# Kernel tuning notes

Hardware: AMD Instinct MI355X
Metric: run time of the kernel (lower is better)

Reference implementation:

```python
import jax, jax.numpy as jnp
import numpy as np

# ---- cfg constants (JDE / YOLOv4-tracking style) ----
STRIDES = (8.0, 16.0, 32.0)
TRAIN_SIZE = 608.0
LEVELS = 3
NUM_ANCHORS = 4
EMB_DIM = 208
CONF_THRESH = 0.5
NMS_IOU = 0.45
K_LEVEL = 300   # proposals kept per level after confidence filtering
MAX_PROP = 500  # final padded proposal count per image
_ANCHORS = np.array([
    [[8, 24], [11, 34], [16, 48], [23, 68]],
    [[32, 96], [45, 135], [64, 192], [90, 271]],
    [[128, 384], [180, 540], [256, 640], [512, 640]],
], dtype=np.float32)  # [LEVELS, NUM_ANCHORS, 2] in pixels


def _decode_level(pred, emb, anchors_px, stride):
    """pred [B,A,H,W,6], emb [B,H,W,E] -> [B, A*H*W, 4+1+E] (xyxy in [0,1], conf, l2-norm emb)."""
    B, A, H, W, _ = pred.shape
    conf = jax.nn.softmax(pred[..., 4:6], axis=-1)[..., 1:2]  # [B,A,H,W,1]
    anc = anchors_px / stride  # anchors in grid units, [A,2]
    gy, gx = jnp.meshgrid(jnp.arange(H, dtype=pred.dtype),
                          jnp.arange(W, dtype=pred.dtype), indexing="ij")
    aw = anc[:, 0][:, None, None]  # [A,1,1]
    ah = anc[:, 1][:, None, None]
    # JDE-style delta decode: offsets scaled by anchor size, exp size decode
    x = pred[..., 0] * aw + gx
    y = pred[..., 1] * ah + gy
    w = jnp.exp(pred[..., 2]) * aw
    h = jnp.exp(pred[..., 3]) * ah
    scale = stride / TRAIN_SIZE  # back to pixels, then normalize by train size
    x1 = jnp.clip((x - 0.5 * w) * scale, 0.0, 1.0)
    y1 = jnp.clip((y - 0.5 * h) * scale, 0.0, 1.0)
    x2 = jnp.clip((x + 0.5 * w) * scale, 0.0, 1.0)
    y2 = jnp.clip((y + 0.5 * h) * scale, 0.0, 1.0)
    box = jnp.stack([x1, y1, x2, y2], axis=-1)  # [B,A,H,W,4]
    # tile embedding over anchors and l2-normalize (tf.math.l2_normalize, eps on sum of squares)
    pe = jnp.broadcast_to(emb[:, None], (B, A, H, W, emb.shape[-1]))
    n2 = jnp.sum(pe * pe, axis=-1, keepdims=True)
    pe = pe * jax.lax.rsqrt(jnp.maximum(n2, 1e-12))
    preds = jnp.concatenate([box, conf, pe], axis=-1)  # [B,A,H,W,4+1+E]
    return preds.reshape(B, A * H * W, preds.shape[-1])


def _conf_topk(props):
    """Confidence threshold + keep top K_LEVEL per image (zero-padded). props [B,N,D]."""
    s = props[..., 4]
    sm = jnp.where(s > CONF_THRESH, s, 0.0)
    top_s, top_i = jax.lax.top_k(sm, K_LEVEL)
    g = jnp.take_along_axis(props, top_i[..., None], axis=1)  # [B,K,D]
    return g * (top_s > 0.0)[..., None].astype(props.dtype)


def _nms_one(props):
    """Greedy NMS for one image. props [N,D] -> [MAX_PROP,D] zero-padded."""
    sc_in = props[:, 4]
    order = jnp.argsort(-sc_in)
    p = props[order]                      # sorted by score desc
    b, sc = p[:, :4], p[:, 4]
    N = b.shape[0]
    area = (b[:, 2] - b[:, 0]) * (b[:, 3] - b[:, 1])
    ix1 = jnp.maximum(b[:, None, 0], b[None, :, 0])
    iy1 = jnp.maximum(b[:, None, 1], b[None, :, 1])
    ix2 = jnp.minimum(b[:, None, 2], b[None, :, 2])
    iy2 = jnp.minimum(b[:, None, 3], b[None, :, 3])
    inter = jnp.clip(ix2 - ix1, 0.0) * jnp.clip(iy2 - iy1, 0.0)
    iou = inter / (area[:, None] + area[None, :] - inter + 1e-9)  # [N,N]
    idxs = jnp.arange(N)
    keep0 = sc > 0.0
    def step(keep, i):
        row = jnp.take(iou, i, axis=0)
        ki = jnp.take(keep, i)
        sup = ki & (row > NMS_IOU) & (idxs > i)
        return keep & jnp.logical_not(sup), None
    keep, _ = jax.lax.scan(step, keep0, idxs)
    keep = keep & (sc > 0.0)
    rank = jnp.cumsum(keep) - 1
    dest = jnp.where(keep & (rank < MAX_PROP), rank, MAX_PROP)  # out-of-range -> dropped
    out = jnp.zeros((MAX_PROP, p.shape[1]), p.dtype).at[dest].set(p, mode="drop")
    return out


def _forward(pred0, pred1, pred2, emb0, emb1, emb2):
    preds = (pred0, pred1, pred2)
    embs = (emb0, emb1, emb2)
    levels = []
    for i in range(LEVELS):
        pr = _decode_level(preds[i], embs[i], jnp.asarray(_ANCHORS[i]), STRIDES[i])
        levels.append(_conf_topk(pr))
    props = jnp.concatenate(levels, axis=1)        # [B, 3*K_LEVEL, 4+1+E]
    out = jax.vmap(_nms_one)(props)                # [B, MAX_PROP, 4+1+E]
    # entry_stop_gradients: grads only through non-zero (valid) entries
    mask = (jnp.sum(out[..., :4], axis=-1) != 0.0).astype(out.dtype)[..., None]
    return out * mask + jax.lax.stop_gradient(out) * (1.0 - mask)


def setup_inputs() -> dict:
    key = jax.random.key(0)
    ks = jax.random.split(key, 6)
    B = 16
    sizes = [76, 38, 19]  # TRAIN_SIZE // stride
    d = {}
    for i, hw in enumerate(sizes):
        d[f"pred{i}"] = jax.random.normal(ks[i], (B, NUM_ANCHORS, hw, hw, 6), jnp.float32)
        d[f"emb{i}"] = jax.random.normal(ks[3 + i], (B, hw, hw, EMB_DIM), jnp.float32)
    return d


def reference(pred0, pred1, pred2, emb0, emb1, emb2):
    return _forward(pred0, pred1, pred2, emb0, emb1, emb2)
```

## Files before the change

### kernel.cpp

```cpp
#include <hip/hip_runtime.h>

typedef unsigned long long u64;
typedef unsigned int u32;

#define KLVL 300
#define NPROP 900
#define MAXPROP 500
#define DDIM 213
#define EDIM 208

__constant__ float c_anc[3][4][2] = {
  {{1.0f, 3.0f}, {1.375f, 4.25f}, {2.0f, 6.0f}, {2.875f, 8.5f}},
  {{2.0f, 6.0f}, {2.8125f, 8.4375f}, {4.0f, 12.0f}, {5.625f, 16.9375f}},
  {{4.0f, 12.0f}, {5.625f, 16.875f}, {8.0f, 20.0f}, {16.0f, 20.0f}},
};
__constant__ float c_scale[3] = { (float)(8.0 / 608.0), (float)(16.0 / 608.0), (float)(32.0 / 608.0) };

__device__ __forceinline__ int level_H(int lvl) { return (lvl == 0) ? 76 : ((lvl == 1) ? 38 : 19); }

#define SB_STRIDE 30336
#define WS_SCORES 0
#define WS_MASK   0
#define MASK_IMG (904*15)
#define WS_SELS (1941504)
#define WS_SELI (WS_SELS + 57600)
#define WS_CNT  (WS_SELI + 57600)
#define WS_BOX  (WS_CNT + 256)
#define BOX_STRIDE 928
#define BOX_IMG (7*928)
#define WS_SRC  (WS_BOX + 415744)

__global__ __launch_bounds__(256) void score_kernel(
    const float* __restrict__ pred0, const float* __restrict__ pred1, const float* __restrict__ pred2,
    float* __restrict__ ws_scores)
{
  const int blk = blockIdx.x;
  const int b = blk / 120;
  const int r = blk % 120;
  int lvl, rb, N, off;
  const float* pred;
  if (r < 91)       { lvl = 0; rb = r;       N = 23104; off = 0;     pred = pred0; }
  else if (r < 114) { lvl = 1; rb = r - 91;  N = 5776;  off = 23104; pred = pred1; }
  else              { lvl = 2; rb = r - 114; N = 1444;  off = 28880; pred = pred2; }
  (void)lvl;
  const int n = rb * 256 + (int)threadIdx.x;
  if (n >= N) return;
  const float* pb = pred + (size_t)b * N * 6;
  float2 l = *reinterpret_cast<const float2*>(pb + (size_t)n * 6 + 4);
  float m = fmaxf(l.x, l.y);
  float e0 = expf(l.x - m), e1 = expf(l.y - m);
  float s = e1 / (e0 + e1);
  ws_scores[(size_t)b * SB_STRIDE + off + n] = (s > 0.5f) ? s : 0.0f;
}

#define TK_T 1024
__global__ __launch_bounds__(TK_T) void select_kernel(
    const float* __restrict__ ws_scores,
    float* __restrict__ sel_score, int* __restrict__ sel_idx, int* __restrict__ cnt)
{
  __shared__ float s_sc[23104];
  __shared__ u32 s_hist[4096];
  __shared__ u32 s_wt[16];
  __shared__ u64 s_wt64[16];
  __shared__ u32 s_sel[4];
  __shared__ float s_selS[KLVL];
  __shared__ int   s_selI[KLVL];

  const int lvl = blockIdx.x % 3;
  const int b = blockIdx.x / 3;
  const int t = threadIdx.x;
  const int lane = t & 63, wid = t >> 6;
  const int H = level_H(lvl);
  const int N = 4 * H * H;
  const int off = (lvl == 0) ? 0 : ((lvl == 1) ? 23104 : 28880);
  const float* gs = ws_scores + (size_t)b * SB_STRIDE + off;

  if (t == 0) s_sel[2] = 0;
  u32 nploc = 0;
  for (int n = t; n < N; n += TK_T) {
    float sm = gs[n];
    s_sc[n] = sm;
    nploc += (sm > 0.0f) ? 1u : 0u;
  }
  __syncthreads();
  if (nploc) atomicAdd(&s_sel[2], nploc);
  __syncthreads();
  const u32 Npos = s_sel[2];
  const bool take_all = (Npos <= (u32)KLVL);
  u32 K = KLVL;
  u32 prefHi = 0, Tkey = 0;

  if (!take_all) {
    for (int pass = 0; pass < 2; ++pass) {
      for (int i = t; i < 4096; i += TK_T) s_hist[i] = 0;
      __syncthreads();
      for (int n = t; n < N; n += TK_T) {
        float v = s_sc[n];
        if (v <= 0.0f) continue;
        u32 key = __float_as_uint(v) - 0x3F000000u;
        if (pass == 0) atomicAdd(&s_hist[key >> 12], 1u);
        else if ((key >> 12) == prefHi) atomicAdd(&s_hist[key & 0xFFFu], 1u);
      }
      __syncthreads();
      const int btop = 4095 - 4 * t;
      u32 h0 = s_hist[btop], h1 = s_hist[btop - 1], h2 = s_hist[btop - 2], h3 = s_hist[btop - 3];
      u32 partial = h0 + h1 + h2 + h3;
      u32 incl = partial;
      #pragma unroll
      for (int off2 = 1; off2 < 64; off2 <<= 1) { u32 v2 = __shfl_up(incl, (unsigned)off2, 64); if (lane >= off2) incl += v2; }
      if (lane == 63) s_wt[wid] = incl;
      __syncthreads();
      u32 above = 0;
      for (int w2 = 0; w2 < wid; ++w2) above += s_wt[w2];
      u32 running = above + incl - partial;
      if (h0 && running < K && K <= running + h0) { s_sel[0] = (u32)(btop);     s_sel[1] = K - running; }
      running += h0;
      if (h1 && running < K && K <= running + h1) { s_sel[0] = (u32)(btop - 1); s_sel[1] = K - running; }
      running += h1;
      if (h2 && running < K && K <= running + h2) { s_sel[0] = (u32)(btop - 2); s_sel[1] = K - running; }
      running += h2;
      if (h3 && running < K && K <= running + h3) { s_sel[0] = (u32)(btop - 3); s_sel[1] = K - running; }
      __syncthreads();
      if (pass == 0) prefHi = s_sel[0];
      else Tkey = (prefHi << 12) | s_sel[0];
      K = s_sel[1];
      __syncthreads();
    }
  }
  const u32 need_ties = take_all ? 0u : K;
  const u32 G = take_all ? Npos : ((u32)KLVL - need_ties);
  const u32 Tbits = Tkey + 0x3F000000u;

  const int chunk = (N + TK_T - 1) / TK_T;
  const int lo = t * chunk;
  const int hi = (lo + chunk < N) ? (lo + chunk) : N;
  u32 cg = 0, ct = 0;
  for (int n = lo; n < hi; ++n) {
    float v = s_sc[n];
    if (v <= 0.0f) continue;
    u32 bits = __float_as_uint(v);
    if (take_all || bits > Tbits) cg++;
    else if (bits == Tbits) ct++;
  }
  u64 pc = ((u64)cg << 32) | (u64)ct;
  u64 incl64 = pc;
  #pragma unroll
  for (int off2 = 1; off2 < 64; off2 <<= 1) { u64 v2 = __shfl_up(incl64, (unsigned)off2, 64); if (lane >= off2) incl64 += v2; }
  if (lane == 63) s_wt64[wid] = incl64;
  __syncthreads();
  u64 ab = 0;
  for (int w2 = 0; w2 < wid; ++w2) ab += s_wt64[w2];
  u64 excl = ab + incl64 - pc;
  u32 g_pos = (u32)(excl >> 32);
  u32 t_pos = (u32)excl;
  for (int n = lo; n < hi; ++n) {
    float v = s_sc[n];
    if (v <= 0.0f) continue;
    u32 bits = __float_as_uint(v);
    if (take_all || bits > Tbits) {
      s_selS[g_pos] = v; s_selI[g_pos] = n; g_pos++;
    } else if (bits == Tbits) {
      if (t_pos < need_ties) { s_selS[G + t_pos] = v; s_selI[G + t_pos] = n; }
      t_pos++;
    }
  }
  __syncthreads();

  const u32 total = take_all ? Npos : (u32)KLVL;
  float* out_s = sel_score + (size_t)b * NPROP + (size_t)lvl * KLVL;
  int* out_i = sel_idx + (size_t)b * NPROP + (size_t)lvl * KLVL;
  if ((u32)t < total) {
    float sv = s_selS[t]; int iv = s_selI[t];
    u32 r = 0;
    for (u32 j = 0; j < total; ++j) {
      float sj = s_selS[j]; int ij = s_selI[j];
      r += ((sj > sv) || (sj == sv && ij < iv)) ? 1u : 0u;
    }
    out_s[r] = sv; out_i[r] = iv;
  }
  for (u32 s2 = total + (u32)t; s2 < (u32)KLVL; s2 += TK_T) { out_s[s2] = 0.0f; out_i[s2] = 0; }
  if (t == 0) cnt[b * 3 + lvl] = (int)total;
}

__global__ __launch_bounds__(1024) void rank_kernel(
    const float* __restrict__ pred0, const float* __restrict__ pred1, const float* __restrict__ pred2,
    const float* __restrict__ sel_score, const int* __restrict__ sel_idx, const int* __restrict__ cnt,
    float* __restrict__ ws_box)
{
  __shared__ float s_sc[NPROP];
  __shared__ int s_ix[NPROP];
  __shared__ int s_c[3];
  const int b = blockIdx.x, t = threadIdx.x;
  if (t < 3) s_c[t] = cnt[b * 3 + t];
  if (t < NPROP) { s_sc[t] = sel_score[(size_t)b * NPROP + t]; s_ix[t] = sel_idx[(size_t)b * NPROP + t]; }
  __syncthreads();
  if (t < NPROP) {
    int lvl = t / KLVL, pos = t - lvl * KLVL;
    if (pos < s_c[lvl]) {
      float sv = s_sc[t];
      u32 rank = (u32)pos;
      for (int ol = 0; ol < 3; ++ol) {
        if (ol == lvl) continue;
        int base = ol * KLVL, co = s_c[ol];
        int lo2 = 0, hi2 = co;
        if (ol < lvl) {
          while (lo2 < hi2) { int mid = (lo2 + hi2) >> 1; if (s_sc[base + mid] >= sv) lo2 = mid + 1; else hi2 = mid; }
        } else {
          while (lo2 < hi2) { int mid = (lo2 + hi2) >> 1; if (s_sc[base + mid] > sv) lo2 = mid + 1; else hi2 = mid; }
        }
        rank += (u32)lo2;
      }
      int n = s_ix[t];
      int Hl = level_H(lvl), HWl = Hl * Hl;
      int a = n / HWl, rem = n - a * HWl, gy = rem / Hl, gx = rem - gy * Hl;
      const float* pred = (lvl == 0) ? pred0 : ((lvl == 1) ? pred1 : pred2);
      const float* p = pred + ((size_t)b * 4 * HWl + (size_t)n) * 6;
      float p0 = p[0], p1 = p[1], p2 = p[2], p3 = p[3];
      float aw = c_anc[lvl][a][0], ah = c_anc[lvl][a][1];
      float x = p0 * aw + (float)gx;
      float y = p1 * ah + (float)gy;
      float wv = expf(p2) * aw;
      float hv = expf(p3) * ah;
      float sc = c_scale[lvl];
      float x1 = fminf(fmaxf((x - 0.5f * wv) * sc, 0.0f), 1.0f);
      float y1 = fminf(fmaxf((y - 0.5f * hv) * sc, 0.0f), 1.0f);
      float x2 = fminf(fmaxf((x + 0.5f * wv) * sc, 0.0f), 1.0f);
      float y2 = fminf(fmaxf((y + 0.5f * hv) * sc, 0.0f), 1.0f);
      float* Bx = ws_box + (size_t)b * BOX_IMG;
      Bx[rank] = x1;
      Bx[BOX_STRIDE + rank] = y1;
      Bx[2 * BOX_STRIDE + rank] = x2;
      Bx[3 * BOX_STRIDE + rank] = y2;
      Bx[4 * BOX_STRIDE + rank] = (x2 - x1) * (y2 - y1);
      Bx[5 * BOX_STRIDE + rank] = sv;
      ((int*)(Bx + 6 * BOX_STRIDE))[rank] = t;
    }
  }
}

__global__ __launch_bounds__(256) void mask_kernel(
    const float* __restrict__ ws_box, const int* __restrict__ cnt, u64* __restrict__ ws_mask)
{
  const int w = blockIdx.x, b = blockIdx.y, t = threadIdx.x;
  const float* B = ws_box + (size_t)b * BOX_IMG;
  const float* X1 = B, * Y1 = B + BOX_STRIDE, * X2 = B + 2 * BOX_STRIDE,
             * Y2 = B + 3 * BOX_STRIDE, * AR = B + 4 * BOX_STRIDE;
  const int Np = cnt[b * 3] + cnt[b * 3 + 1] + cnt[b * 3 + 2];
  __shared__ float jx1[64], jy1[64], jx2[64], jy2[64], jar[64];
  if (t < 64) {
    int j = w * 64 + t;
    if (j < Np) { jx1[t] = X1[j]; jy1[t] = Y1[j]; jx2[t] = X2[j]; jy2[t] = Y2[j]; jar[t] = AR[j]; }
  }
  __syncthreads();
  u64* mk = ws_mask + (size_t)b * MASK_IMG;
  const int jlim = min(64, Np - w * 64);
  for (int i = t; i < Np; i += 256) {
    u64 bits = 0;
    if (i < w * 64 + 63 && jlim > 0) {
      float xi1 = X1[i], yi1 = Y1[i], xi2 = X2[i], yi2 = Y2[i], ai = AR[i];
      for (int jj = 0; jj < jlim; ++jj) {
        int j = w * 64 + jj;
        if (j > i) {
          float xx1 = fmaxf(xi1, jx1[jj]);
          float yy1 = fmaxf(yi1, jy1[jj]);
          float xx2 = fminf(xi2, jx2[jj]);
          float yy2 = fminf(yi2, jy2[jj]);
          float iw = fmaxf(xx2 - xx1, 0.0f);
          float ih = fmaxf(yy2 - yy1, 0.0f);
          float inter = iw * ih;
          float iou = inter / (ai + jar[jj] - inter + 1e-9f);
          if (iou > 0.45f) bits |= (1ull << jj);
        }
      }
    }
    mk[(size_t)i * 15 + w] = bits;
  }
}

__global__ __launch_bounds__(256) void scan_kernel(
    const u64* __restrict__ ws_mask, const int* __restrict__ cnt, int* __restrict__ ws_src)
{
  __shared__ u64 sm[904 * 15];
  __shared__ u64 s_keep[15];
  __shared__ u32 s_pre[16];
  const int b = blockIdx.x, t = threadIdx.x;
  const int Np = cnt[b * 3] + cnt[b * 3 + 1] + cnt[b * 3 + 2];
  const u64* mk = ws_mask + (size_t)b * MASK_IMG;
  for (int i = t; i < Np * 15; i += 256) sm[i] = mk[i];
  __syncthreads();

  if (t < 64) {
    const int lane = t;
    const int lw = (lane < 15) ? lane : 0;
    u64 remv = 0;
    u64 r0 = sm[0 * 15 + lw], r1 = sm[1 * 15 + lw], r2 = sm[2 * 15 + lw], r3 = sm[3 * 15 + lw];
    const int Np4 = Np & ~3;
#define NMS_STEP(ii, rr) { \
      u32 bit_ = (u32)(remv >> ((ii) & 63)) & 1u; \
      u32 sup_ = (u32)__builtin_amdgcn_readlane((int)bit_, (ii) >> 6); \
      if (!sup_) remv |= (rr); }
    for (int i = 0; i < Np4; i += 4) {
      u64 n0 = sm[(size_t)(i + 4) * 15 + lw];
      u64 n1 = sm[(size_t)(i + 5) * 15 + lw];
      u64 n2 = sm[(size_t)(i + 6) * 15 + lw];
      u64 n3 = sm[(size_t)(i + 7) * 15 + lw];
      NMS_STEP(i, r0);
      NMS_STEP(i + 1, r1);
      NMS_STEP(i + 2, r2);
      NMS_STEP(i + 3, r3);
      r0 = n0; r1 = n1; r2 = n2; r3 = n3;
    }
    if (Np4 + 0 < Np) NMS_STEP(Np4 + 0, r0);
    if (Np4 + 1 < Np) NMS_STEP(Np4 + 1, r1);
    if (Np4 + 2 < Np) NMS_STEP(Np4 + 2, r2);
    if (Np4 + 3 < Np) NMS_STEP(Np4 + 3, r3);
#undef NMS_STEP
    if (lane < 15) {
      int base = lane << 6;
      u64 valid = 0;
      if (Np > base) {
        int r = Np - base;
        valid = (r >= 64) ? ~0ull : ((1ull << r) - 1ull);
      }
      s_keep[lane] = (~remv) & valid;
    }
  }
  __syncthreads();
  if (t == 0) {
    u32 run = 0;
    for (int w2 = 0; w2 < 15; ++w2) { s_pre[w2] = run; run += (u32)__popcll(s_keep[w2]); }
  }
  int* src = ws_src + b * MAXPROP;
  for (int r = t; r < MAXPROP; r += 256) src[r] = -1;
  __syncthreads();
  for (int i = t; i < Np; i += 256) {
    u64 kw = s_keep[i >> 6];
    if ((kw >> (i & 63)) & 1ull) {
      u32 rank = s_pre[i >> 6] + (u32)__popcll(kw & ((1ull << (i & 63)) - 1ull));
      if (rank < MAXPROP) src[rank] = i;
    }
  }
}

__global__ __launch_bounds__(256) void out_kernel(
    const float* __restrict__ emb0, const float* __restrict__ emb1, const float* __restrict__ emb2,
    const float* __restrict__ ws_box, const int* __restrict__ ws_src, const int* __restrict__ sel_idx,
    float* __restrict__ out)
{
  const int blk = blockIdx.x;
  const int b = blk / 125;
  const int r = (blk % 125) * 4 + (threadIdx.x >> 6);
  const int lane = threadIdx.x & 63;
  float* orow = out + ((size_t)b * MAXPROP + r) * DDIM;
  const int i = ws_src[b * MAXPROP + r];
  if (i < 0) {
    for (int c = lane; c < DDIM; c += 64) orow[c] = 0.0f;
    return;
  }
  const float* B = ws_box + (size_t)b * BOX_IMG;
  float x1 = B[i], y1 = B[BOX_STRIDE + i], x2 = B[2 * BOX_STRIDE + i], y2 = B[3 * BOX_STRIDE + i];
  float score = B[5 * BOX_STRIDE + i];
  int slot = ((const int*)(B + 6 * BOX_STRIDE))[i];
  int n = sel_idx[(size_t)b * NPROP + slot];
  int lvl = slot / KLVL;
  int Hl = level_H(lvl), HWl = Hl * Hl;
  int a = n / HWl, rem = n - a * HWl, gy = rem / Hl, gx = rem - gy * Hl;
  (void)a;
  const float* emb = (lvl == 0) ? emb0 : ((lvl == 1) ? emb1 : emb2);
  const float* e = emb + ((size_t)(b * Hl + gy) * Hl + gx) * EDIM;
  float v0 = e[lane], v1 = e[lane + 64], v2 = e[lane + 128];
  float v3 = (lane < 16) ? e[lane + 192] : 0.0f;
  float ss = v0 * v0 + v1 * v1 + v2 * v2 + v3 * v3;
  for (int off = 32; off > 0; off >>= 1) ss += __shfl_xor(ss, off, 64);
  float rs = 1.0f / sqrtf(fmaxf(ss, 1e-12f));
  if (lane == 0) {
    orow[0] = x1; orow[1] = y1; orow[2] = x2; orow[3] = y2; orow[4] = score;
  }
  orow[5 + lane] = v0 * rs;
  orow[5 + 64 + lane] = v1 * rs;
  orow[5 + 128 + lane] = v2 * rs;
  if (lane < 16) orow[5 + 192 + lane] = v3 * rs;
}

extern "C" void kernel_launch(void* const* d_in, const int* in_sizes, int n_in,
                              void* d_out, int out_size, void* d_ws, size_t ws_size,
                              hipStream_t stream) {
  const float* pred[3] = {nullptr, nullptr, nullptr};
  const float* emb[3] = {nullptr, nullptr, nullptr};
  for (int i = 0; i < n_in; ++i) {
    const float* p = (const float*)d_in[i];
    switch (in_sizes[i]) {
      case 2217984:  pred[0] = p; break;
      case 554496:   pred[1] = p; break;
      case 138624:   pred[2] = p; break;
      case 19222528: emb[0] = p; break;
      case 4805632:  emb[1] = p; break;
      case 1201408:  emb[2] = p; break;
      default: break;
    }
  }
  char* ws = (char*)d_ws;
  float* ws_scores = (float*)(ws + WS_SCORES);
  u64* ws_mask = (u64*)(ws + WS_MASK);
  float* sel_score = (float*)(ws + WS_SELS);
  int* sel_idx = (int*)(ws + WS_SELI);
  int* cnt = (int*)(ws + WS_CNT);
  float* ws_box = (float*)(ws + WS_BOX);
  int* ws_src = (int*)(ws + WS_SRC);

  score_kernel<<<dim3(1920), dim3(256), 0, stream>>>(pred[0], pred[1], pred[2], ws_scores);
  select_kernel<<<dim3(48), dim3(TK_T), 0, stream>>>(ws_scores, sel_score, sel_idx, cnt);
  rank_kernel<<<dim3(16), dim3(1024), 0, stream>>>(pred[0], pred[1], pred[2], sel_score, sel_idx, cnt, ws_box);
  mask_kernel<<<dim3(15, 16), dim3(256), 0, stream>>>(ws_box, cnt, ws_mask);
  scan_kernel<<<dim3(16), dim3(256), 0, stream>>>(ws_mask, cnt, ws_src);
  out_kernel<<<dim3(2000), dim3(256), 0, stream>>>(emb[0], emb[1], emb[2], ws_box, ws_src, sel_idx, (float*)d_out);
}
```

Before: 270.3 us.

## Replace per-level select with global histogram threshold, collect, and tiled NMS scan

Top-k selection no longer runs in 48 big blocks that each stage a whole level in shared memory. Instead, the score kernel builds a global coarse histogram with atomics, a small kernel finds the threshold bucket, a wide collect kernel gathers candidates, and a sort kernel ranks them. The rank and mask kernels are fused into one, with the mask stored transposed. The NMS scan becomes a single-wave, tile-wise greedy pass using readlane instead of a serial per-box loop. This trades the low-parallelism select and the serial scan for more kernel launches and global atomics, and it depends on capped candidate buffers (512 above the threshold, 1024 tied) that could overflow.

```diff
diff --git a/kernel.cpp b/kernel.cpp
--- a/kernel.cpp
+++ b/kernel.cpp
@@ -19,20 +19,39 @@
 __device__ __forceinline__ int level_H(int lvl) { return (lvl == 0) ? 76 : ((lvl == 1) ? 38 : 19); }
 
 #define SB_STRIDE 30336
-#define WS_SCORES 0
-#define WS_MASK   0
-#define MASK_IMG (904*15)
-#define WS_SELS (1941504)
-#define WS_SELI (WS_SELS + 57600)
-#define WS_CNT  (WS_SELI + 57600)
-#define WS_BOX  (WS_CNT + 256)
+#define MASKT_STRIDE 904
+#define MASK_IMG (15*904)
 #define BOX_STRIDE 928
-#define BOX_IMG (7*928)
-#define WS_SRC  (WS_BOX + 415744)
+#define BOX_IMG (6*928)
+
+#define OFF_SCORES 0
+#define OFF_HIST   1945600
+#define OFF_BUFTS  1945600
+#define OFF_BUFTI  2142208
+#define OFF_BUFGS  2338816
+#define OFF_BUFGI  2437120
+#define OFF_CNTG   2535424
+#define OFF_CNTT   2535680
+#define OFF_THR    2535936
+#define OFF_CNT    2536192
+#define OFF_SELS   2536448
+#define OFF_SELI   2594048
+#define OFF_BOX    2651904
+#define OFF_SRC    3008256
+
+__device__ __forceinline__ u64 readlane_u64(u64 v, int l) {
+  u32 lo = (u32)__builtin_amdgcn_readlane((int)(u32)(v & 0xFFFFFFFFull), l);
+  u32 hi = (u32)__builtin_amdgcn_readlane((int)(u32)(v >> 32), l);
+  return ((u64)hi << 32) | (u64)lo;
+}
+
+__global__ __launch_bounds__(1024) void zero_kernel(u32* __restrict__ h) {
+  h[blockIdx.x * 1024 + threadIdx.x] = 0u;
+}
 
 __global__ __launch_bounds__(256) void score_kernel(
     const float* __restrict__ pred0, const float* __restrict__ pred1, const float* __restrict__ pred2,
-    float* __restrict__ ws_scores)
+    float* __restrict__ ws_scores, u32* __restrict__ hist)
 {
   const int blk = blockIdx.x;
   const int b = blk / 120;
@@ -42,7 +61,6 @@
   if (r < 91)       { lvl = 0; rb = r;       N = 23104; off = 0;     pred = pred0; }
   else if (r < 114) { lvl = 1; rb = r - 91;  N = 5776;  off = 23104; pred = pred1; }
   else              { lvl = 2; rb = r - 114; N = 1444;  off = 28880; pred = pred2; }
-  (void)lvl;
   const int n = rb * 256 + (int)threadIdx.x;
   if (n >= N) return;
   const float* pb = pred + (size_t)b * N * 6;
@@ -50,150 +68,128 @@
   float m = fmaxf(l.x, l.y);
   float e0 = expf(l.x - m), e1 = expf(l.y - m);
   float s = e1 / (e0 + e1);
-  ws_scores[(size_t)b * SB_STRIDE + off + n] = (s > 0.5f) ? s : 0.0f;
-}
-
-#define TK_T 1024
-__global__ __launch_bounds__(TK_T) void select_kernel(
-    const float* __restrict__ ws_scores,
-    float* __restrict__ sel_score, int* __restrict__ sel_idx, int* __restrict__ cnt)
-{
-  __shared__ float s_sc[23104];
-  __shared__ u32 s_hist[4096];
-  __shared__ u32 s_wt[16];
-  __shared__ u64 s_wt64[16];
-  __shared__ u32 s_sel[4];
-  __shared__ float s_selS[KLVL];
-  __shared__ int   s_selI[KLVL];
-
-  const int lvl = blockIdx.x % 3;
-  const int b = blockIdx.x / 3;
-  const int t = threadIdx.x;
-  const int lane = t & 63, wid = t >> 6;
-  const int H = level_H(lvl);
-  const int N = 4 * H * H;
-  const int off = (lvl == 0) ? 0 : ((lvl == 1) ? 23104 : 28880);
-  const float* gs = ws_scores + (size_t)b * SB_STRIDE + off;
-
-  if (t == 0) s_sel[2] = 0;
-  u32 nploc = 0;
-  for (int n = t; n < N; n += TK_T) {
-    float sm = gs[n];
-    s_sc[n] = sm;
-    nploc += (sm > 0.0f) ? 1u : 0u;
-  }
-  __syncthreads();
-  if (nploc) atomicAdd(&s_sel[2], nploc);
-  __syncthreads();
-  const u32 Npos = s_sel[2];
-  const bool take_all = (Npos <= (u32)KLVL);
-  u32 K = KLVL;
-  u32 prefHi = 0, Tkey = 0;
-
-  if (!take_all) {
-    for (int pass = 0; pass < 2; ++pass) {
-      for (int i = t; i < 4096; i += TK_T) s_hist[i] = 0;
-      __syncthreads();
-      for (int n = t; n < N; n += TK_T) {
-        float v = s_sc[n];
-        if (v <= 0.0f) continue;
-        u32 key = __float_as_uint(v) - 0x3F000000u;
-        if (pass == 0) atomicAdd(&s_hist[key >> 12], 1u);
-        else if ((key >> 12) == prefHi) atomicAdd(&s_hist[key & 0xFFFu], 1u);
-      }
-      __syncthreads();
-      const int btop = 4095 - 4 * t;
-      u32 h0 = s_hist[btop], h1 = s_hist[btop - 1], h2 = s_hist[btop - 2], h3 = s_hist[btop - 3];
-      u32 partial = h0 + h1 + h2 + h3;
-      u32 incl = partial;
-      #pragma unroll
-      for (int off2 = 1; off2 < 64; off2 <<= 1) { u32 v2 = __shfl_up(incl, (unsigned)off2, 64); if (lane >= off2) incl += v2; }
-      if (lane == 63) s_wt[wid] = incl;
-      __syncthreads();
-      u32 above = 0;
-      for (int w2 = 0; w2 < wid; ++w2) above += s_wt[w2];
-      u32 running = above + incl - partial;
-      if (h0 && running < K && K <= running + h0) { s_sel[0] = (u32)(btop);     s_sel[1] = K - running; }
-      running += h0;
-      if (h1 && running < K && K <= running + h1) { s_sel[0] = (u32)(btop - 1); s_sel[1] = K - running; }
-      running += h1;
-      if (h2 && running < K && K <= running + h2) { s_sel[0] = (u32)(btop - 2); s_sel[1] = K - running; }
-      running += h2;
-      if (h3 && running < K && K <= running + h3) { s_sel[0] = (u32)(btop - 3); s_sel[1] = K - running; }
-      __syncthreads();
-      if (pass == 0) prefHi = s_sel[0];
-      else Tkey = (prefHi << 12) | s_sel[0];
-      K = s_sel[1];
-      __syncthreads();
+  float sm = (s > 0.5f) ? s : 0.0f;
+  ws_scores[(size_t)b * SB_STRIDE + off + n] = sm;
+  if (sm > 0.0f) {
+    u32 key = __float_as_uint(sm) - 0x3F000000u;
+    u32 bk = min(key >> 12, 2047u);
+    atomicAdd(&hist[(u32)(b * 3 + lvl) * 2048u + bk], 1u);
+  }
+}
+
+__global__ __launch_bounds__(256) void thresh_kernel(
+    const u32* __restrict__ hist, int* __restrict__ thrT, int* __restrict__ cnt,
+    u32* __restrict__ cntG, u32* __restrict__ cntT)
+{
+  __shared__ u32 wt[4];
+  __shared__ int sT;
+  const int bl = blockIdx.x, t = threadIdx.x, lane = t & 63, wid = t >> 6;
+  const u32* h = hist + (size_t)bl * 2048;
+  u32 hv[8]; u32 part = 0;
+  #pragma unroll
+  for (int q = 0; q < 8; ++q) { hv[q] = h[2047 - 8 * t - q]; part += hv[q]; }
+  u32 incl = part;
+  #pragma unroll
+  for (int off = 1; off < 64; off <<= 1) { u32 v = __shfl_up(incl, (unsigned)off, 64); if (lane >= off) incl += v; }
+  if (lane == 63) wt[wid] = incl;
+  __syncthreads();
+  u32 above = 0;
+  for (int w2 = 0; w2 < wid; ++w2) above += wt[w2];
+  const u32 total = wt[0] + wt[1] + wt[2] + wt[3];
+  if (total > 300u) {
+    u32 run = above + incl - part;
+    #pragma unroll
+    for (int q = 0; q < 8; ++q) {
+      u32 hq = hv[q];
+      if (hq && run < 300u && 300u <= run + hq) sT = 2047 - 8 * t - q;
+      run += hq;
     }
   }
-  const u32 need_ties = take_all ? 0u : K;
-  const u32 G = take_all ? Npos : ((u32)KLVL - need_ties);
-  const u32 Tbits = Tkey + 0x3F000000u;
-
-  const int chunk = (N + TK_T - 1) / TK_T;
-  const int lo = t * chunk;
-  const int hi = (lo + chunk < N) ? (lo + chunk) : N;
-  u32 cg = 0, ct = 0;
-  for (int n = lo; n < hi; ++n) {
-    float v = s_sc[n];
-    if (v <= 0.0f) continue;
-    u32 bits = __float_as_uint(v);
-    if (take_all || bits > Tbits) cg++;
-    else if (bits == Tbits) ct++;
-  }
-  u64 pc = ((u64)cg << 32) | (u64)ct;
-  u64 incl64 = pc;
-  #pragma unroll
-  for (int off2 = 1; off2 < 64; off2 <<= 1) { u64 v2 = __shfl_up(incl64, (unsigned)off2, 64); if (lane >= off2) incl64 += v2; }
-  if (lane == 63) s_wt64[wid] = incl64;
-  __syncthreads();
-  u64 ab = 0;
-  for (int w2 = 0; w2 < wid; ++w2) ab += s_wt64[w2];
-  u64 excl = ab + incl64 - pc;
-  u32 g_pos = (u32)(excl >> 32);
-  u32 t_pos = (u32)excl;
-  for (int n = lo; n < hi; ++n) {
-    float v = s_sc[n];
-    if (v <= 0.0f) continue;
-    u32 bits = __float_as_uint(v);
-    if (take_all || bits > Tbits) {
-      s_selS[g_pos] = v; s_selI[g_pos] = n; g_pos++;
-    } else if (bits == Tbits) {
-      if (t_pos < need_ties) { s_selS[G + t_pos] = v; s_selI[G + t_pos] = n; }
-      t_pos++;
-    }
-  }
-  __syncthreads();
-
-  const u32 total = take_all ? Npos : (u32)KLVL;
+  __syncthreads();
+  if (t == 0) {
+    thrT[bl] = (total <= 300u) ? -1 : sT;
+    cnt[bl] = (int)min(total, 300u);
+    cntG[bl] = 0u; cntT[bl] = 0u;
+  }
+}
+
+__global__ __launch_bounds__(256) void collect_kernel(
+    const float* __restrict__ ws_scores, const int* __restrict__ thrT,
+    u32* __restrict__ cntG, u32* __restrict__ cntT,
+    float* __restrict__ bufGs, int* __restrict__ bufGi,
+    float* __restrict__ bufTs, int* __restrict__ bufTi)
+{
+  const int blk = blockIdx.x;
+  const int b = blk / 120;
+  const int r = blk % 120;
+  int lvl, rb, N, off;
+  if (r < 91)       { lvl = 0; rb = r;       N = 23104; off = 0;     }
+  else if (r < 114) { lvl = 1; rb = r - 91;  N = 5776;  off = 23104; }
+  else              { lvl = 2; rb = r - 114; N = 1444;  off = 28880; }
+  const int n = rb * 256 + (int)threadIdx.x;
+  if (n >= N) return;
+  float s = ws_scores[(size_t)b * SB_STRIDE + off + n];
+  if (s <= 0.0f) return;
+  u32 key = __float_as_uint(s) - 0x3F000000u;
+  int bk = (int)min(key >> 12, 2047u);
+  const int bl = b * 3 + lvl;
+  const int T = thrT[bl];
+  if (bk > T) {
+    u32 p = atomicAdd(&cntG[bl], 1u);
+    if (p < 512u) { bufGs[bl * 512 + p] = s; bufGi[bl * 512 + p] = n; }
+  } else if (bk == T) {
+    u32 p = atomicAdd(&cntT[bl], 1u);
+    if (p < 1024u) { bufTs[bl * 1024 + p] = s; bufTi[bl * 1024 + p] = n; }
+  }
+}
+
+__global__ __launch_bounds__(1024) void sort_kernel(
+    const float* __restrict__ bufGs, const int* __restrict__ bufGi,
+    const float* __restrict__ bufTs, const int* __restrict__ bufTi,
+    const u32* __restrict__ cntG, const u32* __restrict__ cntT, const int* __restrict__ cnt,
+    float* __restrict__ sel_score, int* __restrict__ sel_idx)
+{
+  __shared__ float gs[512]; __shared__ int gi[512];
+  __shared__ float ts[1024]; __shared__ int ti[1024];
+  const int bl = blockIdx.x, t = threadIdx.x;
+  const int b = bl / 3, lvl = bl % 3;
+  const int G = (int)min(cntG[bl], 512u);
+  const int Tn = (int)min(cntT[bl], 1024u);
+  const int selCnt = cnt[bl];
+  if (t < G) { gs[t] = bufGs[bl * 512 + t]; gi[t] = bufGi[bl * 512 + t]; }
+  if (t < Tn) { ts[t] = bufTs[bl * 1024 + t]; ti[t] = bufTi[bl * 1024 + t]; }
+  __syncthreads();
   float* out_s = sel_score + (size_t)b * NPROP + (size_t)lvl * KLVL;
   int* out_i = sel_idx + (size_t)b * NPROP + (size_t)lvl * KLVL;
-  if ((u32)t < total) {
-    float sv = s_selS[t]; int iv = s_selI[t];
-    u32 r = 0;
-    for (u32 j = 0; j < total; ++j) {
-      float sj = s_selS[j]; int ij = s_selI[j];
-      r += ((sj > sv) || (sj == sv && ij < iv)) ? 1u : 0u;
-    }
-    out_s[r] = sv; out_i[r] = iv;
-  }
-  for (u32 s2 = total + (u32)t; s2 < (u32)KLVL; s2 += TK_T) { out_s[s2] = 0.0f; out_i[s2] = 0; }
-  if (t == 0) cnt[b * 3 + lvl] = (int)total;
-}
-
-__global__ __launch_bounds__(1024) void rank_kernel(
+  if (t < G) {
+    float sv = gs[t]; int iv = gi[t];
+    int rk = 0;
+    for (int j = 0; j < G; ++j) { float sj = gs[j]; int ij = gi[j]; rk += ((sj > sv) || (sj == sv && ij < iv)) ? 1 : 0; }
+    out_s[rk] = sv; out_i[rk] = iv;
+  }
+  if (t < Tn) {
+    float sv = ts[t]; int iv = ti[t];
+    int rk = 0;
+    for (int j = 0; j < Tn; ++j) { float sj = ts[j]; int ij = ti[j]; rk += ((sj > sv) || (sj == sv && ij < iv)) ? 1 : 0; }
+    if (rk < selCnt - G) { out_s[G + rk] = sv; out_i[G + rk] = iv; }
+  }
+  for (int s2 = selCnt + t; s2 < KLVL; s2 += 1024) { out_s[s2] = 0.0f; out_i[s2] = 0; }
+}
+
+__global__ __launch_bounds__(1024) void rankmask_kernel(
     const float* __restrict__ pred0, const float* __restrict__ pred1, const float* __restrict__ pred2,
     const float* __restrict__ sel_score, const int* __restrict__ sel_idx, const int* __restrict__ cnt,
-    float* __restrict__ ws_box)
+    float* __restrict__ ws_box, u64* __restrict__ ws_mask)
 {
   __shared__ float s_sc[NPROP];
   __shared__ int s_ix[NPROP];
   __shared__ int s_c[3];
+  __shared__ float s_x1[904], s_y1[904], s_x2[904], s_y2[904], s_ar[904];
   const int b = blockIdx.x, t = threadIdx.x;
   if (t < 3) s_c[t] = cnt[b * 3 + t];
   if (t < NPROP) { s_sc[t] = sel_score[(size_t)b * NPROP + t]; s_ix[t] = sel_idx[(size_t)b * NPROP + t]; }
   __syncthreads();
+  const int Np = s_c[0] + s_c[1] + s_c[2];
   if (t < NPROP) {
     int lvl = t / KLVL, pos = t - lvl * KLVL;
     if (pos < s_c[lvl]) {
@@ -231,109 +227,106 @@
       Bx[BOX_STRIDE + rank] = y1;
       Bx[2 * BOX_STRIDE + rank] = x2;
       Bx[3 * BOX_STRIDE + rank] = y2;
-      Bx[4 * BOX_STRIDE + rank] = (x2 - x1) * (y2 - y1);
-      Bx[5 * BOX_STRIDE + rank] = sv;
-      ((int*)(Bx + 6 * BOX_STRIDE))[rank] = t;
+      Bx[4 * BOX_STRIDE + rank] = sv;
+      ((int*)(Bx + 5 * BOX_STRIDE))[rank] = t;
+      s_x1[rank] = x1; s_y1[rank] = y1; s_x2[rank] = x2; s_y2[rank] = y2;
+      s_ar[rank] = (x2 - x1) * (y2 - y1);
     }
   }
-}
-
-__global__ __launch_bounds__(256) void mask_kernel(
-    const float* __restrict__ ws_box, const int* __restrict__ cnt, u64* __restrict__ ws_mask)
-{
-  const int w = blockIdx.x, b = blockIdx.y, t = threadIdx.x;
-  const float* B = ws_box + (size_t)b * BOX_IMG;
-  const float* X1 = B, * Y1 = B + BOX_STRIDE, * X2 = B + 2 * BOX_STRIDE,
-             * Y2 = B + 3 * BOX_STRIDE, * AR = B + 4 * BOX_STRIDE;
-  const int Np = cnt[b * 3] + cnt[b * 3 + 1] + cnt[b * 3 + 2];
-  __shared__ float jx1[64], jy1[64], jx2[64], jy2[64], jar[64];
-  if (t < 64) {
-    int j = w * 64 + t;
-    if (j < Np) { jx1[t] = X1[j]; jy1[t] = Y1[j]; jx2[t] = X2[j]; jy2[t] = Y2[j]; jar[t] = AR[j]; }
-  }
-  __syncthreads();
-  u64* mk = ws_mask + (size_t)b * MASK_IMG;
-  const int jlim = min(64, Np - w * 64);
-  for (int i = t; i < Np; i += 256) {
+  __syncthreads();
+  u64* mkT = ws_mask + (size_t)b * MASK_IMG;
+  const int nW = (Np + 63) >> 6;
+  for (int task = t; task < 15 * 904; task += 1024) {
+    int w = task / 904, i = task - w * 904;
     u64 bits = 0;
-    if (i < w * 64 + 63 && jlim > 0) {
-      float xi1 = X1[i], yi1 = Y1[i], xi2 = X2[i], yi2 = Y2[i], ai = AR[i];
-      for (int jj = 0; jj < jlim; ++jj) {
-        int j = w * 64 + jj;
-        if (j > i) {
-          float xx1 = fmaxf(xi1, jx1[jj]);
-          float yy1 = fmaxf(yi1, jy1[jj]);
-          float xx2 = fminf(xi2, jx2[jj]);
-          float yy2 = fminf(yi2, jy2[jj]);
-          float iw = fmaxf(xx2 - xx1, 0.0f);
-          float ih = fmaxf(yy2 - yy1, 0.0f);
-          float inter = iw * ih;
-          float iou = inter / (ai + jar[jj] - inter + 1e-9f);
-          if (iou > 0.45f) bits |= (1ull << jj);
+    if (i < Np && w < nW) {
+      int j0 = w << 6;
+      int jlim = min(64, Np - j0);
+      if (j0 + 63 > i) {
+        float xi1 = s_x1[i], yi1 = s_y1[i], xi2 = s_x2[i], yi2 = s_y2[i], ai = s_ar[i];
+        for (int jj = 0; jj < jlim; ++jj) {
+          int j = j0 + jj;
+          if (j > i) {
+            float xx1 = fmaxf(xi1, s_x1[j]);
+            float yy1 = fmaxf(yi1, s_y1[j]);
+            float xx2 = fminf(xi2, s_x2[j]);
+            float yy2 = fminf(yi2, s_y2[j]);
+            float iw = fmaxf(xx2 - xx1, 0.0f);
+            float ih = fmaxf(yy2 - yy1, 0.0f);
+            float inter = iw * ih;
+            float iou = inter / (ai + s_ar[j] - inter + 1e-9f);
+            if (iou > 0.45f) bits |= (1ull << jj);
+          }
         }
       }
     }
-    mk[(size_t)i * 15 + w] = bits;
-  }
-}
-
-__global__ __launch_bounds__(256) void scan_kernel(
+    mkT[(size_t)w * MASKT_STRIDE + i] = bits;
+  }
+}
+
+__global__ __launch_bounds__(64) void scan_kernel(
     const u64* __restrict__ ws_mask, const int* __restrict__ cnt, int* __restrict__ ws_src)
 {
-  __shared__ u64 sm[904 * 15];
-  __shared__ u64 s_keep[15];
+  __shared__ u64 s_keep[16];
   __shared__ u32 s_pre[16];
-  const int b = blockIdx.x, t = threadIdx.x;
+  const int b = blockIdx.x;
+  const int lane = (int)threadIdx.x;
   const int Np = cnt[b * 3] + cnt[b * 3 + 1] + cnt[b * 3 + 2];
-  const u64* mk = ws_mask + (size_t)b * MASK_IMG;
-  for (int i = t; i < Np * 15; i += 256) sm[i] = mk[i];
-  __syncthreads();
-
-  if (t < 64) {
-    const int lane = t;
-    const int lw = (lane < 15) ? lane : 0;
-    u64 remv = 0;
-    u64 r0 = sm[0 * 15 + lw], r1 = sm[1 * 15 + lw], r2 = sm[2 * 15 + lw], r3 = sm[3 * 15 + lw];
-    const int Np4 = Np & ~3;
-#define NMS_STEP(ii, rr) { \
-      u32 bit_ = (u32)(remv >> ((ii) & 63)) & 1u; \
-      u32 sup_ = (u32)__builtin_amdgcn_readlane((int)bit_, (ii) >> 6); \
-      if (!sup_) remv |= (rr); }
-    for (int i = 0; i < Np4; i += 4) {
-      u64 n0 = sm[(size_t)(i + 4) * 15 + lw];
-      u64 n1 = sm[(size_t)(i + 5) * 15 + lw];
-      u64 n2 = sm[(size_t)(i + 6) * 15 + lw];
-      u64 n3 = sm[(size_t)(i + 7) * 15 + lw];
-      NMS_STEP(i, r0);
-      NMS_STEP(i + 1, r1);
-      NMS_STEP(i + 2, r2);
-      NMS_STEP(i + 3, r3);
-      r0 = n0; r1 = n1; r2 = n2; r3 = n3;
-    }
-    if (Np4 + 0 < Np) NMS_STEP(Np4 + 0, r0);
-    if (Np4 + 1 < Np) NMS_STEP(Np4 + 1, r1);
-    if (Np4 + 2 < Np) NMS_STEP(Np4 + 2, r2);
-    if (Np4 + 3 < Np) NMS_STEP(Np4 + 3, r3);
-#undef NMS_STEP
-    if (lane < 15) {
-      int base = lane << 6;
-      u64 valid = 0;
-      if (Np > base) {
-        int r = Np - base;
-        valid = (r >= 64) ? ~0ull : ((1ull << r) - 1ull);
-      }
-      s_keep[lane] = (~remv) & valid;
-    }
-  }
-  __syncthreads();
-  if (t == 0) {
-    u32 run = 0;
-    for (int w2 = 0; w2 < 15; ++w2) { s_pre[w2] = run; run += (u32)__popcll(s_keep[w2]); }
-  }
+  const u64* mkT = ws_mask + (size_t)b * MASK_IMG;
+
+#define DECL_DIAG(c) u64 d##c = mkT[(size_t)(c) * MASKT_STRIDE + (c) * 64 + lane];
+  DECL_DIAG(0) DECL_DIAG(1) DECL_DIAG(2) DECL_DIAG(3) DECL_DIAG(4)
+  DECL_DIAG(5) DECL_DIAG(6) DECL_DIAG(7) DECL_DIAG(8) DECL_DIAG(9)
+  DECL_DIAG(10) DECL_DIAG(11) DECL_DIAG(12) DECL_DIAG(13) DECL_DIAG(14)
+#undef DECL_DIAG
+
+  u64 remv = 0;
+  u64 keepw = 0;
+
+#define TILE(c, dvar) \
+  if ((c) * 64 < Np) { \
+    u64 rv = readlane_u64(remv, (c)); \
+    int rem_ = Np - (c) * 64; \
+    u64 valid_ = (rem_ >= 64) ? ~0ull : ((1ull << rem_) - 1ull); \
+    u64 live = valid_ & ~rv; \
+    u64 keep = 0; \
+    while (live) { \
+      int j_ = (int)__builtin_ctzll(live); \
+      keep |= (1ull << j_); \
+      u64 row_ = readlane_u64(dvar, j_); \
+      live &= ~(row_ | (1ull << j_)); \
+    } \
+    if (lane == (c)) keepw = keep; \
+    if (keep && lane > (c) && lane < 15) { \
+      const u64* colw_ = mkT + (size_t)lane * MASKT_STRIDE + (c) * 64; \
+      u64 acc_ = 0; \
+      _Pragma("unroll") \
+      for (int ch_ = 0; ch_ < 8; ++ch_) { \
+        u64 r0_ = colw_[ch_ * 8 + 0], r1_ = colw_[ch_ * 8 + 1], r2_ = colw_[ch_ * 8 + 2], r3_ = colw_[ch_ * 8 + 3]; \
+        u64 r4_ = colw_[ch_ * 8 + 4], r5_ = colw_[ch_ * 8 + 5], r6_ = colw_[ch_ * 8 + 6], r7_ = colw_[ch_ * 8 + 7]; \
+        u32 kb_ = (u32)((keep >> (ch_ * 8)) & 0xFFull); \
+        acc_ |= (kb_ & 1u ? r0_ : 0) | (kb_ & 2u ? r1_ : 0) | (kb_ & 4u ? r2_ : 0) | (kb_ & 8u ? r3_ : 0) \
+              | (kb_ & 16u ? r4_ : 0) | (kb_ & 32u ? r5_ : 0) | (kb_ & 64u ? r6_ : 0) | (kb_ & 128u ? r7_ : 0); \
+      } \
+      remv |= acc_; \
+    } \
+  }
+
+  TILE(0, d0) TILE(1, d1) TILE(2, d2) TILE(3, d3) TILE(4, d4)
+  TILE(5, d5) TILE(6, d6) TILE(7, d7) TILE(8, d8) TILE(9, d9)
+  TILE(10, d10) TILE(11, d11) TILE(12, d12) TILE(13, d13) TILE(14, d14)
+#undef TILE
+
+  u32 pc = (lane < 15) ? (u32)__popcll(keepw) : 0u;
+  u32 incl = pc;
+  #pragma unroll
+  for (int off = 1; off < 64; off <<= 1) { u32 v = __shfl_up(incl, (unsigned)off, 64); if (lane >= off) incl += v; }
+  if (lane < 16) { s_keep[lane] = (lane < 15) ? keepw : 0ull; s_pre[lane] = incl - pc; }
+  __syncthreads();
+
   int* src = ws_src + b * MAXPROP;
-  for (int r = t; r < MAXPROP; r += 256) src[r] = -1;
-  __syncthreads();
-  for (int i = t; i < Np; i += 256) {
+  for (int r = lane; r < MAXPROP; r += 64) src[r] = -1;
+  for (int i = lane; i < Np; i += 64) {
     u64 kw = s_keep[i >> 6];
     if ((kw >> (i & 63)) & 1ull) {
       u32 rank = s_pre[i >> 6] + (u32)__popcll(kw & ((1ull << (i & 63)) - 1ull));
@@ -349,8 +342,8 @@
 {
   const int blk = blockIdx.x;
   const int b = blk / 125;
-  const int r = (blk % 125) * 4 + (threadIdx.x >> 6);
-  const int lane = threadIdx.x & 63;
+  const int r = (blk % 125) * 4 + ((int)threadIdx.x >> 6);
+  const int lane = (int)threadIdx.x & 63;
   float* orow = out + ((size_t)b * MAXPROP + r) * DDIM;
   const int i = ws_src[b * MAXPROP + r];
   if (i < 0) {
@@ -359,8 +352,8 @@
   }
   const float* B = ws_box + (size_t)b * BOX_IMG;
   float x1 = B[i], y1 = B[BOX_STRIDE + i], x2 = B[2 * BOX_STRIDE + i], y2 = B[3 * BOX_STRIDE + i];
-  float score = B[5 * BOX_STRIDE + i];
-  int slot = ((const int*)(B + 6 * BOX_STRIDE))[i];
+  float score = B[4 * BOX_STRIDE + i];
+  int slot = ((const int*)(B + 5 * BOX_STRIDE))[i];
   int n = sel_idx[(size_t)b * NPROP + slot];
   int lvl = slot / KLVL;
   int Hl = level_H(lvl), HWl = Hl * Hl;
@@ -400,18 +393,28 @@
     }
   }
   char* ws = (char*)d_ws;
-  float* ws_scores = (float*)(ws + WS_SCORES);
-  u64* ws_mask = (u64*)(ws + WS_MASK);
-  float* sel_score = (float*)(ws + WS_SELS);
-  int* sel_idx = (int*)(ws + WS_SELI);
-  int* cnt = (int*)(ws + WS_CNT);
-  float* ws_box = (float*)(ws + WS_BOX);
-  int* ws_src = (int*)(ws + WS_SRC);
-
-  score_kernel<<<dim3(1920), dim3(256), 0, stream>>>(pred[0], pred[1], pred[2], ws_scores);
-  select_kernel<<<dim3(48), dim3(TK_T), 0, stream>>>(ws_scores, sel_score, sel_idx, cnt);
-  rank_kernel<<<dim3(16), dim3(1024), 0, stream>>>(pred[0], pred[1], pred[2], sel_score, sel_idx, cnt, ws_box);
-  mask_kernel<<<dim3(15, 16), dim3(256), 0, stream>>>(ws_box, cnt, ws_mask);
-  scan_kernel<<<dim3(16), dim3(256), 0, stream>>>(ws_mask, cnt, ws_src);
+  float* ws_scores = (float*)(ws + OFF_SCORES);
+  u64* ws_mask = (u64*)(ws + OFF_SCORES);
+  u32* hist = (u32*)(ws + OFF_HIST);
+  float* bufTs = (float*)(ws + OFF_BUFTS);
+  int* bufTi = (int*)(ws + OFF_BUFTI);
+  float* bufGs = (float*)(ws + OFF_BUFGS);
+  int* bufGi = (int*)(ws + OFF_BUFGI);
+  u32* cntG = (u32*)(ws + OFF_CNTG);
+  u32* cntT = (u32*)(ws + OFF_CNTT);
+  int* thrT = (int*)(ws + OFF_THR);
+  int* cnt = (int*)(ws + OFF_CNT);
+  float* sel_score = (float*)(ws + OFF_SELS);
+  int* sel_idx = (int*)(ws + OFF_SELI);
+  float* ws_box = (float*)(ws + OFF_BOX);
+  int* ws_src = (int*)(ws + OFF_SRC);
+
+  zero_kernel<<<dim3(96), dim3(1024), 0, stream>>>(hist);
+  score_kernel<<<dim3(1920), dim3(256), 0, stream>>>(pred[0], pred[1], pred[2], ws_scores, hist);
+  thresh_kernel<<<dim3(48), dim3(256), 0, stream>>>(hist, thrT, cnt, cntG, cntT);
+  collect_kernel<<<dim3(1920), dim3(256), 0, stream>>>(ws_scores, thrT, cntG, cntT, bufGs, bufGi, bufTs, bufTi);
+  sort_kernel<<<dim3(48), dim3(1024), 0, stream>>>(bufGs, bufGi, bufTs, bufTi, cntG, cntT, cnt, sel_score, sel_idx);
+  rankmask_kernel<<<dim3(16), dim3(1024), 0, stream>>>(pred[0], pred[1], pred[2], sel_score, sel_idx, cnt, ws_box, ws_mask);
+  scan_kernel<<<dim3(16), dim3(64), 0, stream>>>(ws_mask, cnt, ws_src);
   out_kernel<<<dim3(2000), dim3(256), 0, stream>>>(emb[0], emb[1], emb[2], ws_box, ws_src, sel_idx, (float*)d_out);
 }
```

Result: slower. 357.1 us (+32.1%).
